# Kernel tuning notes

Measured on AMD Instinct MI355X. Metric: run time of the kernel, lower is better.

Reference implementation:

```python
import jax, jax.numpy as jnp
import numpy as np

N, D_IN, D_OUT, B = 200000, 256, 256, 256

def setup_inputs() -> dict:
    key = jax.random.key(0)
    k1, k2, k3, k4, k5 = jax.random.split(key, 5)
    lim = float(np.sqrt(6.0 / (D_IN + D_OUT)))  # xavier_init scale=1
    return {
        "nodes": jax.random.normal(k1, (N, D_IN), dtype=jnp.float32),
        "owner_masks": jax.random.randint(k2, (B, N), 0, 2, dtype=jnp.int32),
        "Wt": jax.random.uniform(k3, (D_OUT, D_IN), jnp.float32, -lim, lim),
        "bt": jax.random.normal(k4, (D_OUT,), dtype=jnp.float32),
        "Wg": jax.random.uniform(k5, (D_OUT, D_IN), jnp.float32, -lim, lim),
        "bg": jnp.ones((D_OUT,), dtype=jnp.float32),  # gate bias init fill_(1)
    }

def reference(nodes, owner_masks, Wt, bt, Wg, bg):
    # gates = sigmoid(Linear(nodes)); data = Linear(nodes)  -> [N, D_OUT]
    gates = jax.nn.sigmoid(nodes @ Wg.T + bg)
    data = nodes @ Wt.T + bt
    # owner-mask matmul == masked scatter-sum over nodes -> [B, D_OUT]
    fmask = owner_masks.astype(jnp.float32)
    res = jnp.einsum('bn,nd->bd', fmask, data * gates)
    return res  # dropout is identity in eval mode
```

## Files before the change

### kernel.cpp

```cpp
#include <hip/hip_runtime.h>
#include <stdint.h>

#define NND 200000

typedef unsigned short u16;
typedef __attribute__((ext_vector_type(4))) float f4;
typedef __attribute__((ext_vector_type(4))) int   i4;
typedef __attribute__((ext_vector_type(2))) unsigned int u2;
typedef __attribute__((ext_vector_type(8))) short s8;
typedef __attribute__((ext_vector_type(4))) float acc4;

__device__ __forceinline__ short f2bf(float f) {
    union { float f; uint32_t u; } v; v.f = f;
    uint32_t r = v.u + 0x7FFFu + ((v.u >> 16) & 1u);
    return (short)(r >> 16);
}
__device__ __forceinline__ uint32_t pack2bf(float a, float b) {
    uint32_t ua = __float_as_uint(a), ub = __float_as_uint(b);
    ua = ua + 0x7FFFu + ((ua >> 16) & 1u);
    ub = ub + 0x7FFFu + ((ub >> 16) & 1u);
    return (ua >> 16) | (ub & 0xFFFF0000u);
}
__device__ __forceinline__ void gld16(const void* g, void* l) {
    __builtin_amdgcn_global_load_lds(
        (const __attribute__((address_space(1))) void*)g,
        (__attribute__((address_space(3))) void*)l, 16, 0, 0);
}

__global__ __launch_bounds__(256) void k_prep(const float* __restrict__ Wt,
                                              const float* __restrict__ Wg,
                                              u16* __restrict__ wtb,
                                              u16* __restrict__ wgb) {
    int i = blockIdx.x * 256 + threadIdx.x;
    wtb[i] = (u16)f2bf(Wt[i]);
    wgb[i] = (u16)f2bf(Wg[i]);
}

__global__ __launch_bounds__(256, 2) void k_h(const float* __restrict__ nodes,
                                              const u16* __restrict__ wtb,
                                              const u16* __restrict__ wgb,
                                              const float* __restrict__ btp,
                                              const float* __restrict__ bgp,
                                              u16* __restrict__ h_t) {
    __shared__ __align__(16) char smem[74752];
    u16* Abf = (u16*)smem;
    u16* Ws0 = (u16*)(smem + 9216);
    u16* Ws1 = (u16*)(smem + 41984);

    const int tid  = threadIdx.x;
    const int lane = tid & 63, wave = tid >> 6;
    const int quad = lane >> 4, l16 = lane & 15;
    const int n0 = blockIdx.x * 64;

    acc4 at_[4][4], ag_[4][4];
#pragma unroll
    for (int rt = 0; rt < 4; ++rt)
#pragma unroll
        for (int dt = 0; dt < 4; ++dt) { at_[rt][dt] = (acc4)0.0f; ag_[rt][dt] = (acc4)0.0f; }

    for (int kt = 0; kt < 4; ++kt) {
        const int k0 = kt * 64;
        f4 av[4];
#pragma unroll
        for (int i = 0; i < 4; ++i) {
            int f = i * 256 + tid;
            int row = f >> 4, kp = f & 15;
            av[i] = *(const f4*)(nodes + (size_t)(n0 + row) * 256 + k0 + kp * 4);
        }
#pragma unroll
        for (int i = 0; i < 8; ++i) {
            int g = i * 256 + tid;
            int dr = g >> 3, c = g & 7;
            size_t off = (size_t)dr * 256 + k0 + ((c ^ (dr & 7)) << 3);
            gld16(wtb + off, Ws0 + g * 8);
            gld16(wgb + off, Ws1 + g * 8);
        }
#pragma unroll
        for (int i = 0; i < 4; ++i) {
            int f = i * 256 + tid;
            int row = f >> 4, kp = f & 15;
            u2 p; p.x = pack2bf(av[i].x, av[i].y); p.y = pack2bf(av[i].z, av[i].w);
            *(u2*)((char*)Abf + row * 144 + kp * 8) = p;
        }
        __syncthreads();
#pragma unroll
        for (int ks = 0; ks < 2; ++ks) {
            s8 af[4];
#pragma unroll
            for (int rt = 0; rt < 4; ++rt)
                af[rt] = *(const s8*)((char*)Abf + (rt * 16 + l16) * 144 + ks * 64 + quad * 16);
#pragma unroll
            for (int dt = 0; dt < 4; ++dt) {
                int dl = wave * 64 + dt * 16 + l16;
                int slot = (ks * 4 + quad) ^ (dl & 7);
                s8 bT = *(const s8*)(Ws0 + dl * 64 + slot * 8);
                s8 bG = *(const s8*)(Ws1 + dl * 64 + slot * 8);
#pragma unroll
                for (int rt = 0; rt < 4; ++rt) {
                    at_[rt][dt] = __builtin_amdgcn_mfma_f32_16x16x32_bf16(af[rt], bT, at_[rt][dt], 0, 0, 0);
                    ag_[rt][dt] = __builtin_amdgcn_mfma_f32_16x16x32_bf16(af[rt], bG, ag_[rt][dt], 0, 0, 0);
                }
            }
        }
        __syncthreads();
    }

    u16* Hs = (u16*)smem;
#pragma unroll
    for (int dt = 0; dt < 4; ++dt) {
        int dl = wave * 64 + dt * 16 + l16;
        float btv = btp[dl], bgv = bgp[dl];
#pragma unroll
        for (int rt = 0; rt < 4; ++rt) {
            float h0, h1, h2, h3;
            float g0 = ag_[rt][dt][0] + bgv, g1 = ag_[rt][dt][1] + bgv;
            float g2 = ag_[rt][dt][2] + bgv, g3 = ag_[rt][dt][3] + bgv;
            h0 = (at_[rt][dt][0] + btv) / (1.0f + __expf(-g0));
            h1 = (at_[rt][dt][1] + btv) / (1.0f + __expf(-g1));
            h2 = (at_[rt][dt][2] + btv) / (1.0f + __expf(-g2));
            h3 = (at_[rt][dt][3] + btv) / (1.0f + __expf(-g3));
            u2 p; p.x = pack2bf(h0, h1); p.y = pack2bf(h2, h3);
            *(u2*)((char*)Hs + dl * 144 + (rt * 16 + quad * 4) * 2) = p;
        }
    }
    __syncthreads();
#pragma unroll
    for (int i = 0; i < 8; ++i) {
        int g = i * 256 + tid;
        int d = g >> 3, c = g & 7;
        f4 v = *(const f4*)((char*)Hs + d * 144 + c * 16);
        *(f4*)(h_t + (size_t)d * NND + n0 + c * 8) = v;
    }
}

__global__ __launch_bounds__(256, 2) void k_res(const int* __restrict__ masks,
                                                const u16* __restrict__ h_t,
                                                float* __restrict__ outp) {
    __shared__ __align__(16) u16 Ms[128 * 64];
    __shared__ __align__(16) u16 Hs[256 * 64];

    const int tid  = threadIdx.x;
    const int lane = tid & 63, wave = tid >> 6;
    const int quad = lane >> 4, l16 = lane & 15;
    const int b0 = blockIdx.x * 128;
    const int wb = wave & 1, wd = wave >> 1;

    acc4 acc[4][8];
#pragma unroll
    for (int rt = 0; rt < 4; ++rt)
#pragma unroll
        for (int dt = 0; dt < 8; ++dt) acc[rt][dt] = (acc4)0.0f;

    for (int it = 0; it < 25; ++it) {
        const int nb = blockIdx.y * 1600 + it * 64;
#pragma unroll
        for (int i = 0; i < 8; ++i) {
            int g = i * 256 + tid;
            int dr = g >> 3, c = g & 7;
            gld16(h_t + (size_t)dr * NND + nb + ((c ^ (dr & 7)) << 3), (char*)Hs + g * 16);
        }
#pragma unroll
        for (int i = 0; i < 4; ++i) {
            int g = i * 256 + tid;
            int dr = g >> 3, c = g & 7;
            const i4* mp = (const i4*)(masks + (size_t)(b0 + dr) * NND + nb + c * 8);
            i4 m0 = mp[0], m1 = mp[1];
            i4 w;
            w.x = (int)((((uint32_t)(-m0.x)) & 0x3F80u) | ((((uint32_t)(-m0.y)) & 0x3F80u) << 16));
            w.y = (int)((((uint32_t)(-m0.z)) & 0x3F80u) | ((((uint32_t)(-m0.w)) & 0x3F80u) << 16));
            w.z = (int)((((uint32_t)(-m1.x)) & 0x3F80u) | ((((uint32_t)(-m1.y)) & 0x3F80u) << 16));
            w.w = (int)((((uint32_t)(-m1.z)) & 0x3F80u) | ((((uint32_t)(-m1.w)) & 0x3F80u) << 16));
            *(i4*)((char*)Ms + dr * 128 + ((c ^ (dr & 7)) << 4)) = w;
        }
        __syncthreads();
#pragma unroll
        for (int ks = 0; ks < 2; ++ks) {
            s8 af[4];
#pragma unroll
            for (int rt = 0; rt < 4; ++rt) {
                int r = wb * 64 + rt * 16 + l16;
                af[rt] = *(const s8*)((char*)Ms + r * 128 + (((ks * 4 + quad) ^ (r & 7)) << 4));
            }
#pragma unroll
            for (int dt = 0; dt < 8; ++dt) {
                int dl = wd * 128 + dt * 16 + l16;
                s8 bf_ = *(const s8*)((char*)Hs + dl * 128 + (((ks * 4 + quad) ^ (dl & 7)) << 4));
#pragma unroll
                for (int rt = 0; rt < 4; ++rt)
                    acc[rt][dt] = __builtin_amdgcn_mfma_f32_16x16x32_bf16(af[rt], bf_, acc[rt][dt], 0, 0, 0);
            }
        }
        __syncthreads();
    }
#pragma unroll
    for (int rt = 0; rt < 4; ++rt)
#pragma unroll
        for (int dt = 0; dt < 8; ++dt) {
            int b = b0 + wb * 64 + rt * 16 + quad * 4;
            int d = wd * 128 + dt * 16 + l16;
#pragma unroll
            for (int r = 0; r < 4; ++r)
                atomicAdd(outp + (size_t)(b + r) * 256 + d, acc[rt][dt][r]);
        }
}

extern "C" void kernel_launch(void* const* d_in, const int* in_sizes, int n_in,
                              void* d_out, int out_size, void* d_ws, size_t ws_size,
                              hipStream_t stream) {
    const float* nodes = (const float*)d_in[0];
    const int*   masks = (const int*)d_in[1];
    const float* Wt    = (const float*)d_in[2];
    const float* bt    = (const float*)d_in[3];
    const float* Wg    = (const float*)d_in[4];
    const float* bg    = (const float*)d_in[5];
    float* outp = (float*)d_out;

    u16* h_t = (u16*)d_ws;
    u16* wtb = (u16*)((char*)d_ws + (size_t)102400000);
    u16* wgb = wtb + 65536;

    hipMemsetAsync(d_out, 0, (size_t)out_size * sizeof(float), stream);
    k_prep<<<dim3(256), dim3(256), 0, stream>>>(Wt, Wg, wtb, wgb);
    k_h<<<dim3(3125), dim3(256), 0, stream>>>(nodes, wtb, wgb, bt, bg, h_t);
    k_res<<<dim3(2, 125), dim3(256), 0, stream>>>(masks, h_t, outp);
}
```

Before: 523.9 us.

## Use 512-thread blocks, finer N split, and register-prefetch mask tiles

Both GEMM kernels move to 512-thread blocks, so each wave owns a smaller output tile and holds fewer accumulators. k_res splits N into 209 chunks of 960 instead of 125 chunks of 1600, giving more blocks and more parallelism. It also prefetches the next mask tile into registers while the MFMAs run. k_h swizzles the A tile layout in LDS and drops one barrier per K step. The cost is more atomicAdd traffic on the output and higher register and LDS pressure per CU.

```diff
diff --git a/kernel.cpp b/kernel.cpp
--- a/kernel.cpp
+++ b/kernel.cpp
@@ -21,6 +21,7 @@
     ub = ub + 0x7FFFu + ((ub >> 16) & 1u);
     return (ua >> 16) | (ub & 0xFFFF0000u);
 }
+__device__ __forceinline__ float bf2f(uint32_t s) { return __uint_as_float(s << 16); }
 __device__ __forceinline__ void gld16(const void* g, void* l) {
     __builtin_amdgcn_global_load_lds(
         (const __attribute__((address_space(1))) void*)g,
@@ -36,7 +37,7 @@
     wgb[i] = (u16)f2bf(Wg[i]);
 }
 
-__global__ __launch_bounds__(256, 2) void k_h(const float* __restrict__ nodes,
+__global__ __launch_bounds__(512, 4) void k_h(const float* __restrict__ nodes,
                                               const u16* __restrict__ wtb,
                                               const u16* __restrict__ wgb,
                                               const float* __restrict__ btp,
@@ -44,57 +45,55 @@
                                               u16* __restrict__ h_t) {
     __shared__ __align__(16) char smem[74752];
     u16* Abf = (u16*)smem;
-    u16* Ws0 = (u16*)(smem + 9216);
-    u16* Ws1 = (u16*)(smem + 41984);
+    u16* Ws  = (u16*)(smem + 9216);
+    u16* Hs  = (u16*)smem;
 
     const int tid  = threadIdx.x;
     const int lane = tid & 63, wave = tid >> 6;
     const int quad = lane >> 4, l16 = lane & 15;
     const int n0 = blockIdx.x * 64;
-
-    acc4 at_[4][4], ag_[4][4];
+    const int arow = tid >> 3, aslot = tid & 7;
+
+    acc4 at_[4][2], ag_[4][2];
 #pragma unroll
     for (int rt = 0; rt < 4; ++rt)
 #pragma unroll
-        for (int dt = 0; dt < 4; ++dt) { at_[rt][dt] = (acc4)0.0f; ag_[rt][dt] = (acc4)0.0f; }
+        for (int dt = 0; dt < 2; ++dt) { at_[rt][dt] = (acc4)0.0f; ag_[rt][dt] = (acc4)0.0f; }
 
     for (int kt = 0; kt < 4; ++kt) {
         const int k0 = kt * 64;
-        f4 av[4];
+        const float* ap = nodes + (size_t)(n0 + arow) * 256 + k0 + aslot * 8;
+        f4 a0 = ((const f4*)ap)[0];
+        f4 a1 = ((const f4*)ap)[1];
+        if (kt) __syncthreads();
 #pragma unroll
         for (int i = 0; i < 4; ++i) {
-            int f = i * 256 + tid;
-            int row = f >> 4, kp = f & 15;
-            av[i] = *(const f4*)(nodes + (size_t)(n0 + row) * 256 + k0 + kp * 4);
-        }
-#pragma unroll
-        for (int i = 0; i < 8; ++i) {
-            int g = i * 256 + tid;
+            int g = i * 512 + tid;
             int dr = g >> 3, c = g & 7;
             size_t off = (size_t)dr * 256 + k0 + ((c ^ (dr & 7)) << 3);
-            gld16(wtb + off, Ws0 + g * 8);
-            gld16(wgb + off, Ws1 + g * 8);
-        }
-#pragma unroll
-        for (int i = 0; i < 4; ++i) {
-            int f = i * 256 + tid;
-            int row = f >> 4, kp = f & 15;
-            u2 p; p.x = pack2bf(av[i].x, av[i].y); p.y = pack2bf(av[i].z, av[i].w);
-            *(u2*)((char*)Abf + row * 144 + kp * 8) = p;
+            gld16(wtb + off, (char*)Ws + g * 16);
+            gld16(wgb + off, (char*)Ws + 32768 + g * 16);
+        }
+        {
+            i4 aw;
+            aw.x = (int)pack2bf(a0.x, a0.y); aw.y = (int)pack2bf(a0.z, a0.w);
+            aw.z = (int)pack2bf(a1.x, a1.y); aw.w = (int)pack2bf(a1.z, a1.w);
+            *(i4*)((char*)Abf + arow * 144 + ((aslot ^ (arow & 7)) << 4)) = aw;
         }
         __syncthreads();
 #pragma unroll
         for (int ks = 0; ks < 2; ++ks) {
+            const int q = (ks << 2) | quad;
             s8 af[4];
 #pragma unroll
             for (int rt = 0; rt < 4; ++rt)
-                af[rt] = *(const s8*)((char*)Abf + (rt * 16 + l16) * 144 + ks * 64 + quad * 16);
-#pragma unroll
-            for (int dt = 0; dt < 4; ++dt) {
-                int dl = wave * 64 + dt * 16 + l16;
-                int slot = (ks * 4 + quad) ^ (dl & 7);
-                s8 bT = *(const s8*)(Ws0 + dl * 64 + slot * 8);
-                s8 bG = *(const s8*)(Ws1 + dl * 64 + slot * 8);
+                af[rt] = *(const s8*)((char*)Abf + (rt * 16 + l16) * 144 + ((q ^ (l16 & 7)) << 4));
+#pragma unroll
+            for (int dt = 0; dt < 2; ++dt) {
+                int dl = wave * 32 + dt * 16 + l16;
+                int sl = (q ^ (dl & 7)) << 4;
+                s8 bT = *(const s8*)((char*)Ws + dl * 128 + sl);
+                s8 bG = *(const s8*)((char*)Ws + 32768 + dl * 128 + sl);
 #pragma unroll
                 for (int rt = 0; rt < 4; ++rt) {
                     at_[rt][dt] = __builtin_amdgcn_mfma_f32_16x16x32_bf16(af[rt], bT, at_[rt][dt], 0, 0, 0);
@@ -102,89 +101,103 @@
                 }
             }
         }
-        __syncthreads();
-    }
-
-    u16* Hs = (u16*)smem;
-#pragma unroll
-    for (int dt = 0; dt < 4; ++dt) {
-        int dl = wave * 64 + dt * 16 + l16;
+    }
+    __syncthreads();
+
+#pragma unroll
+    for (int dt = 0; dt < 2; ++dt) {
+        int dl = wave * 32 + dt * 16 + l16;
         float btv = btp[dl], bgv = bgp[dl];
 #pragma unroll
         for (int rt = 0; rt < 4; ++rt) {
-            float h0, h1, h2, h3;
-            float g0 = ag_[rt][dt][0] + bgv, g1 = ag_[rt][dt][1] + bgv;
-            float g2 = ag_[rt][dt][2] + bgv, g3 = ag_[rt][dt][3] + bgv;
-            h0 = (at_[rt][dt][0] + btv) / (1.0f + __expf(-g0));
-            h1 = (at_[rt][dt][1] + btv) / (1.0f + __expf(-g1));
-            h2 = (at_[rt][dt][2] + btv) / (1.0f + __expf(-g2));
-            h3 = (at_[rt][dt][3] + btv) / (1.0f + __expf(-g3));
+            float h0 = (at_[rt][dt][0] + btv) / (1.0f + __expf(-(ag_[rt][dt][0] + bgv)));
+            float h1 = (at_[rt][dt][1] + btv) / (1.0f + __expf(-(ag_[rt][dt][1] + bgv)));
+            float h2 = (at_[rt][dt][2] + btv) / (1.0f + __expf(-(ag_[rt][dt][2] + bgv)));
+            float h3 = (at_[rt][dt][3] + btv) / (1.0f + __expf(-(ag_[rt][dt][3] + bgv)));
             u2 p; p.x = pack2bf(h0, h1); p.y = pack2bf(h2, h3);
             *(u2*)((char*)Hs + dl * 144 + (rt * 16 + quad * 4) * 2) = p;
         }
     }
     __syncthreads();
 #pragma unroll
-    for (int i = 0; i < 8; ++i) {
-        int g = i * 256 + tid;
+    for (int i = 0; i < 4; ++i) {
+        int g = i * 512 + tid;
         int d = g >> 3, c = g & 7;
         f4 v = *(const f4*)((char*)Hs + d * 144 + c * 16);
         *(f4*)(h_t + (size_t)d * NND + n0 + c * 8) = v;
     }
 }
 
-__global__ __launch_bounds__(256, 2) void k_res(const int* __restrict__ masks,
+__global__ __launch_bounds__(512, 4) void k_res(const int* __restrict__ masks,
                                                 const u16* __restrict__ h_t,
                                                 float* __restrict__ outp) {
-    __shared__ __align__(16) u16 Ms[128 * 64];
-    __shared__ __align__(16) u16 Hs[256 * 64];
+    __shared__ __align__(16) char smem[49152];
+    u16* Ms = (u16*)smem;
+    u16* Hs = (u16*)(smem + 16384);
 
     const int tid  = threadIdx.x;
     const int lane = tid & 63, wave = tid >> 6;
     const int quad = lane >> 4, l16 = lane & 15;
+    const int bh = wave & 1, dq = wave >> 1;
     const int b0 = blockIdx.x * 128;
-    const int wb = wave & 1, wd = wave >> 1;
-
-    acc4 acc[4][8];
+    const int nbase = blockIdx.y * 960;
+    const int R = min(15, (NND - nbase) / 64);
+
+    acc4 acc[4][4];
 #pragma unroll
     for (int rt = 0; rt < 4; ++rt)
 #pragma unroll
-        for (int dt = 0; dt < 8; ++dt) acc[rt][dt] = (acc4)0.0f;
-
-    for (int it = 0; it < 25; ++it) {
-        const int nb = blockIdx.y * 1600 + it * 64;
-#pragma unroll
-        for (int i = 0; i < 8; ++i) {
-            int g = i * 256 + tid;
+        for (int dt = 0; dt < 4; ++dt) acc[rt][dt] = (acc4)0.0f;
+
+    const int mr0 = tid >> 3, mc0 = tid & 7;
+    const int mr1 = (512 + tid) >> 3, mc1 = tid & 7;
+    i4 mp[2][2];
+    {
+        const i4* p0 = (const i4*)(masks + (size_t)(b0 + mr0) * NND + nbase + mc0 * 8);
+        const i4* p1 = (const i4*)(masks + (size_t)(b0 + mr1) * NND + nbase + mc1 * 8);
+        mp[0][0] = p0[0]; mp[0][1] = p0[1];
+        mp[1][0] = p1[0]; mp[1][1] = p1[1];
+    }
+
+    for (int it = 0; it < R; ++it) {
+        const int nb = nbase + it * 64;
+#pragma unroll
+        for (int i = 0; i < 4; ++i) {
+            int g = i * 512 + tid;
             int dr = g >> 3, c = g & 7;
             gld16(h_t + (size_t)dr * NND + nb + ((c ^ (dr & 7)) << 3), (char*)Hs + g * 16);
         }
 #pragma unroll
-        for (int i = 0; i < 4; ++i) {
-            int g = i * 256 + tid;
-            int dr = g >> 3, c = g & 7;
-            const i4* mp = (const i4*)(masks + (size_t)(b0 + dr) * NND + nb + c * 8);
-            i4 m0 = mp[0], m1 = mp[1];
+        for (int i = 0; i < 2; ++i) {
+            int mr = (i == 0) ? mr0 : mr1, c = (i == 0) ? mc0 : mc1;
             i4 w;
-            w.x = (int)((((uint32_t)(-m0.x)) & 0x3F80u) | ((((uint32_t)(-m0.y)) & 0x3F80u) << 16));
-            w.y = (int)((((uint32_t)(-m0.z)) & 0x3F80u) | ((((uint32_t)(-m0.w)) & 0x3F80u) << 16));
-            w.z = (int)((((uint32_t)(-m1.x)) & 0x3F80u) | ((((uint32_t)(-m1.y)) & 0x3F80u) << 16));
-            w.w = (int)((((uint32_t)(-m1.z)) & 0x3F80u) | ((((uint32_t)(-m1.w)) & 0x3F80u) << 16));
-            *(i4*)((char*)Ms + dr * 128 + ((c ^ (dr & 7)) << 4)) = w;
+            w.x = (int)((((uint32_t)(-mp[i][0].x)) & 0x3F80u) | ((((uint32_t)(-mp[i][0].y)) & 0x3F80u) << 16));
+            w.y = (int)((((uint32_t)(-mp[i][0].z)) & 0x3F80u) | ((((uint32_t)(-mp[i][0].w)) & 0x3F80u) << 16));
+            w.z = (int)((((uint32_t)(-mp[i][1].x)) & 0x3F80u) | ((((uint32_t)(-mp[i][1].y)) & 0x3F80u) << 16));
+            w.w = (int)((((uint32_t)(-mp[i][1].z)) & 0x3F80u) | ((((uint32_t)(-mp[i][1].w)) & 0x3F80u) << 16));
+            *(i4*)((char*)Ms + mr * 128 + ((c ^ (mr & 7)) << 4)) = w;
         }
         __syncthreads();
+        if (it + 1 < R) {
+            const int nn = nb + 64;
+            const i4* p0 = (const i4*)(masks + (size_t)(b0 + mr0) * NND + nn + mc0 * 8);
+            const i4* p1 = (const i4*)(masks + (size_t)(b0 + mr1) * NND + nn + mc1 * 8);
+            mp[0][0] = p0[0]; mp[0][1] = p0[1];
+            mp[1][0] = p1[0]; mp[1][1] = p1[1];
+        }
 #pragma unroll
         for (int ks = 0; ks < 2; ++ks) {
+            const int q = (ks << 2) | quad;
             s8 af[4];
 #pragma unroll
             for (int rt = 0; rt < 4; ++rt) {
-                int r = wb * 64 + rt * 16 + l16;
-                af[rt] = *(const s8*)((char*)Ms + r * 128 + (((ks * 4 + quad) ^ (r & 7)) << 4));
+                int r = bh * 64 + rt * 16 + l16;
+                af[rt] = *(const s8*)((char*)Ms + r * 128 + ((q ^ (l16 & 7)) << 4));
             }
 #pragma unroll
-            for (int dt = 0; dt < 8; ++dt) {
-                int dl = wd * 128 + dt * 16 + l16;
-                s8 bf_ = *(const s8*)((char*)Hs + dl * 128 + (((ks * 4 + quad) ^ (dl & 7)) << 4));
+            for (int dt = 0; dt < 4; ++dt) {
+                int dl = dq * 64 + dt * 16 + l16;
+                s8 bf_ = *(const s8*)((char*)Hs + dl * 128 + ((q ^ (dl & 7)) << 4));
 #pragma unroll
                 for (int rt = 0; rt < 4; ++rt)
                     acc[rt][dt] = __builtin_amdgcn_mfma_f32_16x16x32_bf16(af[rt], bf_, acc[rt][dt], 0, 0, 0);
@@ -195,9 +208,9 @@
 #pragma unroll
     for (int rt = 0; rt < 4; ++rt)
 #pragma unroll
-        for (int dt = 0; dt < 8; ++dt) {
-            int b = b0 + wb * 64 + rt * 16 + quad * 4;
-            int d = wd * 128 + dt * 16 + l16;
+        for (int dt = 0; dt < 4; ++dt) {
+            int b = b0 + bh * 64 + rt * 16 + quad * 4;
+            int d = dq * 64 + dt * 16 + l16;
 #pragma unroll
             for (int r = 0; r < 4; ++r)
                 atomicAdd(outp + (size_t)(b + r) * 256 + d, acc[rt][dt][r]);
@@ -221,6 +234,6 @@
 
     hipMemsetAsync(d_out, 0, (size_t)out_size * sizeof(float), stream);
     k_prep<<<dim3(256), dim3(256), 0, stream>>>(Wt, Wg, wtb, wgb);
-    k_h<<<dim3(3125), dim3(256), 0, stream>>>(nodes, wtb, wgb, bt, bg, h_t);
-    k_res<<<dim3(2, 125), dim3(256), 0, stream>>>(masks, h_t, outp);
-}
+    k_h<<<dim3(3125), dim3(512), 0, stream>>>(nodes, wtb, wgb, bt, bg, h_t);
+    k_res<<<dim3(2, 209), dim3(512), 0, stream>>>(masks, h_t, outp);
+}
```

Measured after the change: 501.7 us. 4.2% less time.

## Retile mask-matmul kernel to 64 rows, prefetch masks, swizzle A tiles in LDS

Applied to the files above, without the earlier changes.

The mask-weighted reduction kernel now uses 64-row batch tiles with 4x4 accumulators per wave, runs more blocks (4x157) and raises occupancy to 3 blocks per CU. It prefetches the next mask tile into registers while the current MFMA step runs. Both kernels gain an XOR-swizzled LDS layout for the A operand to cut bank conflicts, and the projection kernel drops one barrier per k-step. In exchange, each H tile is reloaded by twice as many blocks, and the larger grid produces more atomic adds on the output.

```diff
diff --git a/kernel.cpp b/kernel.cpp
--- a/kernel.cpp
+++ b/kernel.cpp
@@ -44,8 +44,8 @@
                                               u16* __restrict__ h_t) {
     __shared__ __align__(16) char smem[74752];
     u16* Abf = (u16*)smem;
-    u16* Ws0 = (u16*)(smem + 9216);
-    u16* Ws1 = (u16*)(smem + 41984);
+    char* Ws = smem + 9216;
+    u16* Hs  = (u16*)smem;
 
     const int tid  = threadIdx.x;
     const int lane = tid & 63, wave = tid >> 6;
@@ -63,38 +63,40 @@
         f4 av[4];
 #pragma unroll
         for (int i = 0; i < 4; ++i) {
-            int f = i * 256 + tid;
-            int row = f >> 4, kp = f & 15;
-            av[i] = *(const f4*)(nodes + (size_t)(n0 + row) * 256 + k0 + kp * 4);
-        }
+            int g = i * 256 + tid;
+            int row = g >> 4, col = g & 15;
+            av[i] = *(const f4*)(nodes + (size_t)(n0 + row) * 256 + k0 + col * 4);
+        }
+        if (kt) __syncthreads();
 #pragma unroll
         for (int i = 0; i < 8; ++i) {
             int g = i * 256 + tid;
             int dr = g >> 3, c = g & 7;
             size_t off = (size_t)dr * 256 + k0 + ((c ^ (dr & 7)) << 3);
-            gld16(wtb + off, Ws0 + g * 8);
-            gld16(wgb + off, Ws1 + g * 8);
-        }
-#pragma unroll
-        for (int i = 0; i < 4; ++i) {
-            int f = i * 256 + tid;
-            int row = f >> 4, kp = f & 15;
+            gld16(wtb + off, Ws + g * 16);
+            gld16(wgb + off, Ws + 32768 + g * 16);
+        }
+#pragma unroll
+        for (int i = 0; i < 4; ++i) {
+            int g = i * 256 + tid;
+            int row = g >> 4, col = g & 15;
             u2 p; p.x = pack2bf(av[i].x, av[i].y); p.y = pack2bf(av[i].z, av[i].w);
-            *(u2*)((char*)Abf + row * 144 + kp * 8) = p;
+            *(u2*)((char*)Abf + row * 144 + (((col >> 1) ^ (row & 7)) << 4) + (col & 1) * 8) = p;
         }
         __syncthreads();
 #pragma unroll
         for (int ks = 0; ks < 2; ++ks) {
+            const int q = (ks << 2) | quad;
             s8 af[4];
 #pragma unroll
             for (int rt = 0; rt < 4; ++rt)
-                af[rt] = *(const s8*)((char*)Abf + (rt * 16 + l16) * 144 + ks * 64 + quad * 16);
+                af[rt] = *(const s8*)((char*)Abf + (rt * 16 + l16) * 144 + ((q ^ (l16 & 7)) << 4));
 #pragma unroll
             for (int dt = 0; dt < 4; ++dt) {
                 int dl = wave * 64 + dt * 16 + l16;
-                int slot = (ks * 4 + quad) ^ (dl & 7);
-                s8 bT = *(const s8*)(Ws0 + dl * 64 + slot * 8);
-                s8 bG = *(const s8*)(Ws1 + dl * 64 + slot * 8);
+                int sl = (q ^ (dl & 7)) << 4;
+                s8 bT = *(const s8*)(Ws + dl * 128 + sl);
+                s8 bG = *(const s8*)(Ws + 32768 + dl * 128 + sl);
 #pragma unroll
                 for (int rt = 0; rt < 4; ++rt) {
                     at_[rt][dt] = __builtin_amdgcn_mfma_f32_16x16x32_bf16(af[rt], bT, at_[rt][dt], 0, 0, 0);
@@ -102,23 +104,19 @@
                 }
             }
         }
-        __syncthreads();
-    }
-
-    u16* Hs = (u16*)smem;
+    }
+    __syncthreads();
+
 #pragma unroll
     for (int dt = 0; dt < 4; ++dt) {
         int dl = wave * 64 + dt * 16 + l16;
         float btv = btp[dl], bgv = bgp[dl];
 #pragma unroll
         for (int rt = 0; rt < 4; ++rt) {
-            float h0, h1, h2, h3;
-            float g0 = ag_[rt][dt][0] + bgv, g1 = ag_[rt][dt][1] + bgv;
-            float g2 = ag_[rt][dt][2] + bgv, g3 = ag_[rt][dt][3] + bgv;
-            h0 = (at_[rt][dt][0] + btv) / (1.0f + __expf(-g0));
-            h1 = (at_[rt][dt][1] + btv) / (1.0f + __expf(-g1));
-            h2 = (at_[rt][dt][2] + btv) / (1.0f + __expf(-g2));
-            h3 = (at_[rt][dt][3] + btv) / (1.0f + __expf(-g3));
+            float h0 = (at_[rt][dt][0] + btv) / (1.0f + __expf(-(ag_[rt][dt][0] + bgv)));
+            float h1 = (at_[rt][dt][1] + btv) / (1.0f + __expf(-(ag_[rt][dt][1] + bgv)));
+            float h2 = (at_[rt][dt][2] + btv) / (1.0f + __expf(-(ag_[rt][dt][2] + bgv)));
+            float h3 = (at_[rt][dt][3] + btv) / (1.0f + __expf(-(ag_[rt][dt][3] + bgv)));
             u2 p; p.x = pack2bf(h0, h1); p.y = pack2bf(h2, h3);
             *(u2*)((char*)Hs + dl * 144 + (rt * 16 + quad * 4) * 2) = p;
         }
@@ -133,58 +131,75 @@
     }
 }
 
-__global__ __launch_bounds__(256, 2) void k_res(const int* __restrict__ masks,
+__global__ __launch_bounds__(256, 3) void k_res(const int* __restrict__ masks,
                                                 const u16* __restrict__ h_t,
                                                 float* __restrict__ outp) {
-    __shared__ __align__(16) u16 Ms[128 * 64];
-    __shared__ __align__(16) u16 Hs[256 * 64];
+    __shared__ __align__(16) char smem[41984];
+    u16* Ms = (u16*)smem;
+    char* Hsc = smem + 9216;
 
     const int tid  = threadIdx.x;
     const int lane = tid & 63, wave = tid >> 6;
     const int quad = lane >> 4, l16 = lane & 15;
-    const int b0 = blockIdx.x * 128;
-    const int wb = wave & 1, wd = wave >> 1;
-
-    acc4 acc[4][8];
+    const int b0 = blockIdx.x * 64;
+    const int t0 = blockIdx.y * 20;
+    const int R = min(20, 3125 - t0);
+
+    acc4 acc[4][4];
 #pragma unroll
     for (int rt = 0; rt < 4; ++rt)
 #pragma unroll
-        for (int dt = 0; dt < 8; ++dt) acc[rt][dt] = (acc4)0.0f;
-
-    for (int it = 0; it < 25; ++it) {
-        const int nb = blockIdx.y * 1600 + it * 64;
+        for (int dt = 0; dt < 4; ++dt) acc[rt][dt] = (acc4)0.0f;
+
+    i4 mp[4];
+    {
+        const int nb0 = t0 * 64;
+#pragma unroll
+        for (int i = 0; i < 4; ++i) {
+            int g = i * 256 + tid;
+            int row = g >> 4, seg = g & 15;
+            mp[i] = *(const i4*)(masks + (size_t)(b0 + row) * NND + nb0 + seg * 4);
+        }
+    }
+
+    for (int it = 0; it < R; ++it) {
+        const int nb = (t0 + it) * 64;
 #pragma unroll
         for (int i = 0; i < 8; ++i) {
             int g = i * 256 + tid;
             int dr = g >> 3, c = g & 7;
-            gld16(h_t + (size_t)dr * NND + nb + ((c ^ (dr & 7)) << 3), (char*)Hs + g * 16);
-        }
-#pragma unroll
-        for (int i = 0; i < 4; ++i) {
-            int g = i * 256 + tid;
-            int dr = g >> 3, c = g & 7;
-            const i4* mp = (const i4*)(masks + (size_t)(b0 + dr) * NND + nb + c * 8);
-            i4 m0 = mp[0], m1 = mp[1];
-            i4 w;
-            w.x = (int)((((uint32_t)(-m0.x)) & 0x3F80u) | ((((uint32_t)(-m0.y)) & 0x3F80u) << 16));
-            w.y = (int)((((uint32_t)(-m0.z)) & 0x3F80u) | ((((uint32_t)(-m0.w)) & 0x3F80u) << 16));
-            w.z = (int)((((uint32_t)(-m1.x)) & 0x3F80u) | ((((uint32_t)(-m1.y)) & 0x3F80u) << 16));
-            w.w = (int)((((uint32_t)(-m1.z)) & 0x3F80u) | ((((uint32_t)(-m1.w)) & 0x3F80u) << 16));
-            *(i4*)((char*)Ms + dr * 128 + ((c ^ (dr & 7)) << 4)) = w;
+            gld16(h_t + (size_t)dr * NND + nb + ((c ^ (dr & 7)) << 3), Hsc + g * 16);
+        }
+#pragma unroll
+        for (int i = 0; i < 4; ++i) {
+            int g = i * 256 + tid;
+            int row = g >> 4, seg = g & 15;
+            u2 w;
+            w.x = (((uint32_t)(-mp[i].x)) & 0x3F80u) | ((((uint32_t)(-mp[i].y)) & 0x3F80u) << 16);
+            w.y = (((uint32_t)(-mp[i].z)) & 0x3F80u) | ((((uint32_t)(-mp[i].w)) & 0x3F80u) << 16);
+            *(u2*)((char*)Ms + row * 144 + (((seg >> 1) ^ (row & 7)) << 4) + (seg & 1) * 8) = w;
         }
         __syncthreads();
+        if (it + 1 < R) {
+            const int nn = nb + 64;
+#pragma unroll
+            for (int i = 0; i < 4; ++i) {
+                int g = i * 256 + tid;
+                int row = g >> 4, seg = g & 15;
+                mp[i] = *(const i4*)(masks + (size_t)(b0 + row) * NND + nn + seg * 4);
+            }
+        }
 #pragma unroll
         for (int ks = 0; ks < 2; ++ks) {
+            const int q = (ks << 2) | quad;
             s8 af[4];
 #pragma unroll
-            for (int rt = 0; rt < 4; ++rt) {
-                int r = wb * 64 + rt * 16 + l16;
-                af[rt] = *(const s8*)((char*)Ms + r * 128 + (((ks * 4 + quad) ^ (r & 7)) << 4));
-            }
-#pragma unroll
-            for (int dt = 0; dt < 8; ++dt) {
-                int dl = wd * 128 + dt * 16 + l16;
-                s8 bf_ = *(const s8*)((char*)Hs + dl * 128 + (((ks * 4 + quad) ^ (dl & 7)) << 4));
+            for (int rt = 0; rt < 4; ++rt)
+                af[rt] = *(const s8*)((char*)Ms + (rt * 16 + l16) * 144 + ((q ^ (l16 & 7)) << 4));
+#pragma unroll
+            for (int dt = 0; dt < 4; ++dt) {
+                int dl = wave * 64 + dt * 16 + l16;
+                s8 bf_ = *(const s8*)(Hsc + dl * 128 + ((q ^ (dl & 7)) << 4));
 #pragma unroll
                 for (int rt = 0; rt < 4; ++rt)
                     acc[rt][dt] = __builtin_amdgcn_mfma_f32_16x16x32_bf16(af[rt], bf_, acc[rt][dt], 0, 0, 0);
@@ -195,9 +210,9 @@
 #pragma unroll
     for (int rt = 0; rt < 4; ++rt)
 #pragma unroll
-        for (int dt = 0; dt < 8; ++dt) {
-            int b = b0 + wb * 64 + rt * 16 + quad * 4;
-            int d = wd * 128 + dt * 16 + l16;
+        for (int dt = 0; dt < 4; ++dt) {
+            int b = b0 + rt * 16 + quad * 4;
+            int d = wave * 64 + dt * 16 + l16;
 #pragma unroll
             for (int r = 0; r < 4; ++r)
                 atomicAdd(outp + (size_t)(b + r) * 256 + d, acc[rt][dt][r]);
@@ -222,5 +237,5 @@
     hipMemsetAsync(d_out, 0, (size_t)out_size * sizeof(float), stream);
     k_prep<<<dim3(256), dim3(256), 0, stream>>>(Wt, Wg, wtb, wgb);
     k_h<<<dim3(3125), dim3(256), 0, stream>>>(nodes, wtb, wgb, bt, bg, h_t);
-    k_res<<<dim3(2, 125), dim3(256), 0, stream>>>(masks, h_t, outp);
-}
+    k_res<<<dim3(4, 157), dim3(256), 0, stream>>>(masks, h_t, outp);
+}
```

Result: no change. 518.5 us (-1.0%).
